# Kernel tuning notes

Measured on AMD Instinct MI355X. Metric: run time of the kernel, lower is better.

The kernel has to match this reference:

```python
import jax, jax.numpy as jnp
import numpy as np

N = 50000
D = 128
E = 640000


def _sage_conv(x, src, dst, w_self, w_neigh, b, n_nodes):
    # DGL SAGEConv(aggregator_type='mean'):
    #   h_neigh = mean_{u in N(v)} x_u ; out = x @ W_self + h_neigh @ W_neigh + b
    msg = x[src]                                          # [E, D] irregular gather
    s = jax.ops.segment_sum(msg, dst, num_segments=n_nodes)   # [N, D]
    deg = jax.ops.segment_sum(jnp.ones((src.shape[0],), dtype=x.dtype), dst,
                              num_segments=n_nodes)       # [N]
    h_neigh = jnp.where(deg[:, None] > 0, s / jnp.maximum(deg, 1.0)[:, None], 0.0)
    return x @ w_self + h_neigh @ w_neigh + b


def setup_inputs() -> dict:
    key = jax.random.key(0)
    ks = jax.random.split(key, 16)
    feat = jax.random.normal(ks[0], (N, D), dtype=jnp.float32)
    src = jax.random.randint(ks[1], (E,), 0, N, dtype=jnp.int32)
    dst = jax.random.randint(ks[2], (E,), 0, N, dtype=jnp.int32)
    etype = jax.random.randint(ks[3], (E,), 0, 4, dtype=jnp.int32)
    scale = 1.0 / np.sqrt(D)
    inp = {"feat": feat, "src": src, "dst": dst, "etype": etype}
    for i, name in enumerate(["1", "2", "3"]):
        inp[f"w_self{name}"] = jax.random.normal(ks[4 + 3 * i], (D, D), dtype=jnp.float32) * scale
        inp[f"w_neigh{name}"] = jax.random.normal(ks[5 + 3 * i], (D, D), dtype=jnp.float32) * scale
        inp[f"b{name}"] = jnp.zeros((D,), dtype=jnp.float32)
    return inp


def reference(feat, src, dst, etype,
              w_self1, w_neigh1, b1,
              w_self2, w_neigh2, b2,
              w_self3, w_neigh3, b3):
    n = feat.shape[0]
    h = _sage_conv(feat, src, dst, w_self1, w_neigh1, b1, n)
    h = jax.nn.relu(h) + feat
    h_prev = h
    h = _sage_conv(h, src, dst, w_self2, w_neigh2, b2, n)
    h = jax.nn.relu(h) + h_prev
    h_prev = h
    h = _sage_conv(h, src, dst, w_self3, w_neigh3, b3, n)
    h = jax.nn.relu(h) + h_prev
    return h
```

## Files before the change

### kernel.cpp

```cpp
#include <hip/hip_runtime.h>


#define DFEAT 128
#define BUCKET_CAP 64

typedef unsigned short ushort_t;
typedef unsigned int uint_t;
using short8  = __attribute__((ext_vector_type(8))) short;
using floatx4 = __attribute__((ext_vector_type(4))) float;

static __device__ __forceinline__ ushort_t f2bf(float f) {
    unsigned int u = __float_as_uint(f);
    u = (u + 0x7fffu + ((u >> 16) & 1u)) >> 16;
    return (ushort_t)u;
}
static __device__ __forceinline__ float bflo(uint_t v) {
    return __uint_as_float(v << 16);
}
static __device__ __forceinline__ float bfhi(uint_t v) {
    return __uint_as_float(v & 0xffff0000u);
}
static __device__ __forceinline__ float bf2f(ushort_t u) {
    return __uint_as_float((uint_t)u << 16);
}

__global__ void fill_buckets(const int* __restrict__ src, const int* __restrict__ dst,
                             int* __restrict__ cnt, ushort_t* __restrict__ bucket, int E) {
    int i = blockIdx.x * blockDim.x + threadIdx.x;
    if (i >= E) return;
    int d = dst[i];
    int slot = atomicAdd(&cnt[d], 1);
    if (slot < BUCKET_CAP) bucket[(size_t)d * BUCKET_CAP + slot] = (ushort_t)src[i];
}

__global__ __launch_bounds__(256) void prep_all(const float* __restrict__ w0,
                                                const float* __restrict__ w1,
                                                const float* __restrict__ w2,
                                                const float* __restrict__ w3,
                                                const float* __restrict__ w4,
                                                const float* __restrict__ w5,
                                                ushort_t* __restrict__ wt,
                                                const float* __restrict__ feat,
                                                ushort_t* __restrict__ featb,
                                                int* __restrict__ cnt,
                                                int n, int zb) {
    int b = blockIdx.x;
    if (b < zb) {
        int i = b * 1024 + threadIdx.x * 4;
        if (i < n) *(int4*)&cnt[i] = make_int4(0, 0, 0, 0);
        return;
    }
    b -= zb;
    if (b < 384) {
        const float* ws[6] = {w0, w1, w2, w3, w4, w5};
        const float* W = ws[b >> 6];
        ushort_t* O = wt + (size_t)(b >> 6) * DFEAT * DFEAT;
        int idx = (b & 63) * 256 + threadIdx.x;
        int k = idx >> 7, nn = idx & 127;
        O[nn * DFEAT + k] = f2bf(W[idx]);
        return;
    }
    b -= 384;
    int i = b * 256 + threadIdx.x;
    const float4* p = (const float4*)feat + (size_t)2 * i;
    float4 v0 = p[0], v1 = p[1];
    short8 u;
    u[0] = (short)f2bf(v0.x); u[1] = (short)f2bf(v0.y);
    u[2] = (short)f2bf(v0.z); u[3] = (short)f2bf(v0.w);
    u[4] = (short)f2bf(v1.x); u[5] = (short)f2bf(v1.y);
    u[6] = (short)f2bf(v1.z); u[7] = (short)f2bf(v1.w);
    *(short8*)&featb[(size_t)i * 8] = u;
}

__global__ __launch_bounds__(256) void aggregate(const ushort_t* __restrict__ xb,
                                                 const int* __restrict__ cnt,
                                                 const ushort_t* __restrict__ bucket,
                                                 ushort_t* __restrict__ outb, int n) {
    int node = (int)((blockIdx.x * blockDim.x + threadIdx.x) >> 6);
    int lane = threadIdx.x & 63;
    if (node >= n) return;
    int cn = cnt[node];
    int m = cn < BUCKET_CAP ? cn : BUCKET_CAP;
    const ushort_t* bk = bucket + (size_t)node * BUCKET_CAP;
    int myidx = (lane < m) ? (int)bk[lane] : 0;
    const uint_t* x1 = (const uint_t*)xb;

    float sx[8], sy[8];
#pragma unroll
    for (int j = 0; j < 8; ++j) { sx[j] = 0.f; sy[j] = 0.f; }

#pragma unroll 1
    for (int i = 0; i < m; i += 8) {
        int s[8];
#pragma unroll
        for (int j = 0; j < 8; ++j) s[j] = __shfl(myidx, i + j);
#pragma unroll
        for (int j = 1; j < 8; ++j) s[j] = (i + j < m) ? s[j] : s[0];
        uint_t v[8];
#pragma unroll
        for (int j = 0; j < 8; ++j) v[j] = x1[(size_t)s[j] * 64 + lane];
        sx[0] += bflo(v[0]); sy[0] += bfhi(v[0]);
#pragma unroll
        for (int j = 1; j < 8; ++j) {
            if (i + j < m) { sx[j] += bflo(v[j]); sy[j] += bfhi(v[j]); }
        }
    }
    float tx = ((sx[0] + sx[1]) + (sx[2] + sx[3])) + ((sx[4] + sx[5]) + (sx[6] + sx[7]));
    float ty = ((sy[0] + sy[1]) + (sy[2] + sy[3])) + ((sy[4] + sy[5]) + (sy[6] + sy[7]));
    float inv = cn > 0 ? 1.0f / (float)cn : 0.0f;
    uint_t o = ((uint_t)f2bf(ty * inv) << 16) | (uint_t)f2bf(tx * inv);
    ((uint_t*)outb)[(size_t)node * 64 + lane] = o;
}

__global__ __launch_bounds__(256) void sage_gemm_mfma(const ushort_t* __restrict__ xb,
                                                      const ushort_t* __restrict__ nbb,
                                                      const ushort_t* __restrict__ WsT,
                                                      const ushort_t* __restrict__ WnT,
                                                      const float* __restrict__ bias,
                                                      float* __restrict__ outf,
                                                      ushort_t* __restrict__ outb, int n) {
    __shared__ ushort_t As[64 * DFEAT];
    int t = threadIdx.x;
    int lane = t & 63;
    int w = t >> 6;
    int lr = lane & 15;
    int lg = lane >> 4;
    int row0 = blockIdx.x * 64;

    floatx4 acc[4][2];
#pragma unroll
    for (int m = 0; m < 4; ++m)
#pragma unroll
        for (int tt = 0; tt < 2; ++tt) acc[m][tt] = (floatx4)0.f;

#pragma unroll 1
    for (int phase = 0; phase < 2; ++phase) {
        const ushort_t* A = phase ? xb : nbb;
        const ushort_t* W = phase ? WsT : WnT;
        __syncthreads();
#pragma unroll
        for (int i = 0; i < 4; ++i) {
            int slot = i * 256 + t;
            int r = slot >> 4;
            int c = slot & 15;
            int gr = row0 + r;
            short8 u = (short8)0;
            if (gr < n) u = *(const short8*)&A[(size_t)gr * DFEAT + c * 8];
            int sc = c ^ (r & 7);
            *(short8*)&As[r * DFEAT + sc * 8] = u;
        }
        __syncthreads();
#pragma unroll
        for (int s = 0; s < 4; ++s) {
            short8 a[4], b[2];
#pragma unroll
            for (int m = 0; m < 4; ++m) {
                int r = m * 16 + lr;
                int c = s * 4 + lg;
                int sc = c ^ (r & 7);
                a[m] = *(const short8*)&As[r * DFEAT + sc * 8];
            }
#pragma unroll
            for (int tt = 0; tt < 2; ++tt) {
                int nn = w * 32 + tt * 16 + lr;
                b[tt] = *(const short8*)&W[(size_t)nn * DFEAT + s * 32 + lg * 8];
            }
#pragma unroll
            for (int m = 0; m < 4; ++m)
#pragma unroll
                for (int tt = 0; tt < 2; ++tt)
                    acc[m][tt] = __builtin_amdgcn_mfma_f32_16x16x32_bf16(
                        a[m], b[tt], acc[m][tt], 0, 0, 0);
        }
    }
#pragma unroll
    for (int tt = 0; tt < 2; ++tt) {
        int col = w * 32 + tt * 16 + lr;
        float bb = bias[col];
        int cch = col >> 3, cel = col & 7;
#pragma unroll
        for (int m = 0; m < 4; ++m) {
#pragma unroll
            for (int j = 0; j < 4; ++j) {
                int r = m * 16 + lg * 4 + j;
                int gr = row0 + r;
                if (gr < n) {
                    float xr = bf2f(As[r * DFEAT + (cch ^ (r & 7)) * 8 + cel]);
                    float v = fmaxf(acc[m][tt][j] + bb, 0.f) + xr;
                    if (outf) outf[(size_t)gr * DFEAT + col] = v;
                    if (outb) outb[(size_t)gr * DFEAT + col] = f2bf(v);
                }
            }
        }
    }
}

extern "C" void kernel_launch(void* const* d_in, const int* in_sizes, int n_in,
                              void* d_out, int out_size, void* d_ws, size_t ws_size,
                              hipStream_t stream) {
    const float* feat = (const float*)d_in[0];
    const int*   src  = (const int*)d_in[1];
    const int*   dst  = (const int*)d_in[2];
    const float* Ws1 = (const float*)d_in[4];
    const float* Wn1 = (const float*)d_in[5];
    const float* b1  = (const float*)d_in[6];
    const float* Ws2 = (const float*)d_in[7];
    const float* Wn2 = (const float*)d_in[8];
    const float* b2  = (const float*)d_in[9];
    const float* Ws3 = (const float*)d_in[10];
    const float* Wn3 = (const float*)d_in[11];
    const float* b3  = (const float*)d_in[12];

    int n = in_sizes[0] / DFEAT;
    int E = in_sizes[1];

    char* ws = (char*)d_ws;
    size_t off = 0;
    auto alloc = [&](size_t bytes) {
        size_t o = off;
        off = (off + bytes + 255) & ~(size_t)255;
        return o;
    };
    int*      cnt    = (int*)(ws + alloc((size_t)n * sizeof(int)));
    ushort_t* bucket = (ushort_t*)(ws + alloc((size_t)n * BUCKET_CAP * sizeof(ushort_t)));
    ushort_t* neighb = (ushort_t*)(ws + alloc((size_t)n * DFEAT * sizeof(ushort_t)));
    ushort_t* featb  = (ushort_t*)(ws + alloc((size_t)n * DFEAT * sizeof(ushort_t)));
    ushort_t* h1b    = (ushort_t*)(ws + alloc((size_t)n * DFEAT * sizeof(ushort_t)));
    ushort_t* Wt     = (ushort_t*)(ws + alloc((size_t)6 * DFEAT * DFEAT * sizeof(ushort_t)));
    ushort_t* h2b    = featb;
    (void)ws_size;

    ushort_t* Ws1T = Wt + 0 * DFEAT * DFEAT;
    ushort_t* Wn1T = Wt + 1 * DFEAT * DFEAT;
    ushort_t* Ws2T = Wt + 2 * DFEAT * DFEAT;
    ushort_t* Wn2T = Wt + 3 * DFEAT * DFEAT;
    ushort_t* Ws3T = Wt + 4 * DFEAT * DFEAT;
    ushort_t* Wn3T = Wt + 5 * DFEAT * DFEAT;

    float* outp = (float*)d_out;

    int zb = (n + 1023) / 1024;
    int cv = (n * DFEAT / 8 + 255) / 256;
    prep_all<<<zb + 384 + cv, 256, 0, stream>>>(Ws1, Wn1, Ws2, Wn2, Ws3, Wn3, Wt,
                                                feat, featb, cnt, n, zb);
    fill_buckets<<<(E + 255) / 256, 256, 0, stream>>>(src, dst, cnt, bucket, E);

    int agg_blocks  = (n + 3) / 4;
    int gemm_blocks = (n + 63) / 64;

    aggregate<<<agg_blocks, 256, 0, stream>>>(featb, cnt, bucket, neighb, n);
    sage_gemm_mfma<<<gemm_blocks, 256, 0, stream>>>(featb, neighb, Ws1T, Wn1T, b1,
                                                    nullptr, h1b, n);
    aggregate<<<agg_blocks, 256, 0, stream>>>(h1b, cnt, bucket, neighb, n);
    sage_gemm_mfma<<<gemm_blocks, 256, 0, stream>>>(h1b, neighb, Ws2T, Wn2T, b2,
                                                    nullptr, h2b, n);
    aggregate<<<agg_blocks, 256, 0, stream>>>(h2b, cnt, bucket, neighb, n);
    sage_gemm_mfma<<<gemm_blocks, 256, 0, stream>>>(h2b, neighb, Ws3T, Wn3T, b3,
                                                    outp, nullptr, n);
}
```

Baseline: 185.7 us.

## Build compact CSR adjacency and fuse mean aggregation into the MFMA GEMM kernel

Replaces fixed-capacity per-node buckets with a compact CSR built by histogram, wave-level scan with atomic range allocation, and scatter. Each GEMM block now gathers and averages neighbour features for its 64 rows directly into shared memory before running both MFMA products, removing the separate aggregate kernel and the neighbour-feature round trip through global memory. It also handles degrees above 64 exactly. In exchange, the gather runs with far fewer waves in flight (16 nodes per wave sequentially), and the CSR build adds an extra pass over the edges.

```diff
diff --git a/kernel.cpp b/kernel.cpp
--- a/kernel.cpp
+++ b/kernel.cpp
@@ -2,7 +2,6 @@
 
 
 #define DFEAT 128
-#define BUCKET_CAP 64
 
 typedef unsigned short ushort_t;
 typedef unsigned int uint_t;
@@ -14,24 +13,9 @@
     u = (u + 0x7fffu + ((u >> 16) & 1u)) >> 16;
     return (ushort_t)u;
 }
-static __device__ __forceinline__ float bflo(uint_t v) {
-    return __uint_as_float(v << 16);
-}
-static __device__ __forceinline__ float bfhi(uint_t v) {
-    return __uint_as_float(v & 0xffff0000u);
-}
-static __device__ __forceinline__ float bf2f(ushort_t u) {
-    return __uint_as_float((uint_t)u << 16);
-}
-
-__global__ void fill_buckets(const int* __restrict__ src, const int* __restrict__ dst,
-                             int* __restrict__ cnt, ushort_t* __restrict__ bucket, int E) {
-    int i = blockIdx.x * blockDim.x + threadIdx.x;
-    if (i >= E) return;
-    int d = dst[i];
-    int slot = atomicAdd(&cnt[d], 1);
-    if (slot < BUCKET_CAP) bucket[(size_t)d * BUCKET_CAP + slot] = (ushort_t)src[i];
-}
+static __device__ __forceinline__ float bflo(uint_t v) { return __uint_as_float(v << 16); }
+static __device__ __forceinline__ float bfhi(uint_t v) { return __uint_as_float(v & 0xffff0000u); }
+static __device__ __forceinline__ float bf2f(ushort_t u) { return __uint_as_float((uint_t)u << 16); }
 
 __global__ __launch_bounds__(256) void prep_all(const float* __restrict__ w0,
                                                 const float* __restrict__ w1,
@@ -43,11 +27,11 @@
                                                 const float* __restrict__ feat,
                                                 ushort_t* __restrict__ featb,
                                                 int* __restrict__ cnt,
-                                                int n, int zb) {
+                                                int nz, int zb) {
     int b = blockIdx.x;
     if (b < zb) {
         int i = b * 1024 + threadIdx.x * 4;
-        if (i < n) *(int4*)&cnt[i] = make_int4(0, 0, 0, 0);
+        if (i < nz) *(int4*)&cnt[i] = make_int4(0, 0, 0, 0);
         return;
     }
     b -= zb;
@@ -72,54 +56,54 @@
     *(short8*)&featb[(size_t)i * 8] = u;
 }
 
-__global__ __launch_bounds__(256) void aggregate(const ushort_t* __restrict__ xb,
-                                                 const int* __restrict__ cnt,
-                                                 const ushort_t* __restrict__ bucket,
-                                                 ushort_t* __restrict__ outb, int n) {
-    int node = (int)((blockIdx.x * blockDim.x + threadIdx.x) >> 6);
+__global__ void hist_k(const int* __restrict__ dst, int* __restrict__ cnt, int E) {
+    int i = blockIdx.x * blockDim.x + threadIdx.x;
+    if (i < E) atomicAdd(&cnt[dst[i]], 1);
+}
+
+__global__ __launch_bounds__(256) void alloc_ranges(const int* __restrict__ cnt,
+                                                    int2* __restrict__ meta,
+                                                    int* __restrict__ cursor,
+                                                    int* __restrict__ gcur, int n) {
+    int node = blockIdx.x * 256 + threadIdx.x;
     int lane = threadIdx.x & 63;
-    if (node >= n) return;
-    int cn = cnt[node];
-    int m = cn < BUCKET_CAP ? cn : BUCKET_CAP;
-    const ushort_t* bk = bucket + (size_t)node * BUCKET_CAP;
-    int myidx = (lane < m) ? (int)bk[lane] : 0;
-    const uint_t* x1 = (const uint_t*)xb;
-
-    float sx[8], sy[8];
-#pragma unroll
-    for (int j = 0; j < 8; ++j) { sx[j] = 0.f; sy[j] = 0.f; }
-
-#pragma unroll 1
-    for (int i = 0; i < m; i += 8) {
-        int s[8];
-#pragma unroll
-        for (int j = 0; j < 8; ++j) s[j] = __shfl(myidx, i + j);
-#pragma unroll
-        for (int j = 1; j < 8; ++j) s[j] = (i + j < m) ? s[j] : s[0];
-        uint_t v[8];
-#pragma unroll
-        for (int j = 0; j < 8; ++j) v[j] = x1[(size_t)s[j] * 64 + lane];
-        sx[0] += bflo(v[0]); sy[0] += bfhi(v[0]);
-#pragma unroll
-        for (int j = 1; j < 8; ++j) {
-            if (i + j < m) { sx[j] += bflo(v[j]); sy[j] += bfhi(v[j]); }
-        }
-    }
-    float tx = ((sx[0] + sx[1]) + (sx[2] + sx[3])) + ((sx[4] + sx[5]) + (sx[6] + sx[7]));
-    float ty = ((sy[0] + sy[1]) + (sy[2] + sy[3])) + ((sy[4] + sy[5]) + (sy[6] + sy[7]));
-    float inv = cn > 0 ? 1.0f / (float)cn : 0.0f;
-    uint_t o = ((uint_t)f2bf(ty * inv) << 16) | (uint_t)f2bf(tx * inv);
-    ((uint_t*)outb)[(size_t)node * 64 + lane] = o;
-}
-
-__global__ __launch_bounds__(256) void sage_gemm_mfma(const ushort_t* __restrict__ xb,
-                                                      const ushort_t* __restrict__ nbb,
-                                                      const ushort_t* __restrict__ WsT,
-                                                      const ushort_t* __restrict__ WnT,
-                                                      const float* __restrict__ bias,
-                                                      float* __restrict__ outf,
-                                                      ushort_t* __restrict__ outb, int n) {
+    int deg = (node < n) ? cnt[node] : 0;
+    int incl = deg;
+#pragma unroll
+    for (int d = 1; d < 64; d <<= 1) {
+        int v = __shfl_up(incl, d);
+        if (lane >= d) incl += v;
+    }
+    int total = __shfl(incl, 63);
+    int base = 0;
+    if (lane == 63 && total > 0) base = atomicAdd(gcur, total);
+    base = __shfl(base, 63);
+    int start = base + incl - deg;
+    if (node < n) {
+        meta[node] = make_int2(start, deg);
+        cursor[node] = start;
+    }
+}
+
+__global__ void scatter_csr(const int* __restrict__ src, const int* __restrict__ dst,
+                            int* __restrict__ cursor, ushort_t* __restrict__ csr, int E) {
+    int i = blockIdx.x * blockDim.x + threadIdx.x;
+    if (i >= E) return;
+    int d = dst[i];
+    int pos = atomicAdd(&cursor[d], 1);
+    csr[pos] = (ushort_t)src[i];
+}
+
+__global__ __launch_bounds__(256) void sage_fused(const ushort_t* __restrict__ xb,
+                                                  const int2* __restrict__ meta,
+                                                  const ushort_t* __restrict__ csr,
+                                                  const ushort_t* __restrict__ WsT,
+                                                  const ushort_t* __restrict__ WnT,
+                                                  const float* __restrict__ bias,
+                                                  float* __restrict__ outf,
+                                                  ushort_t* __restrict__ outb, int n) {
     __shared__ ushort_t As[64 * DFEAT];
+    __shared__ ushort_t Nb[64 * DFEAT];
     int t = threadIdx.x;
     int lane = t & 63;
     int w = t >> 6;
@@ -127,52 +111,122 @@
     int lg = lane >> 4;
     int row0 = blockIdx.x * 64;
 
+#pragma unroll
+    for (int i = 0; i < 4; ++i) {
+        int slot = i * 256 + t;
+        int r = slot >> 4;
+        int c = slot & 15;
+        int gr = row0 + r;
+        short8 u = (short8)0;
+        if (gr < n) u = *(const short8*)&xb[(size_t)gr * DFEAT + c * 8];
+        *(short8*)&As[r * DFEAT + (c ^ (r & 7)) * 8] = u;
+    }
+
+    const uint_t* x1 = (const uint_t*)xb;
+    int nbase = row0 + w * 16;
+    int cn_n = 0, bs_n = 0, ix_n = 0;
+    if (nbase < n) {
+        int2 md = meta[nbase];
+        cn_n = md.y; bs_n = md.x;
+        int mm = cn_n < 64 ? cn_n : 64;
+        ix_n = (lane < mm) ? (int)csr[bs_n + lane] : 0;
+    }
+#pragma unroll 1
+    for (int i = 0; i < 16; ++i) {
+        int node = nbase + i;
+        int cn = cn_n, base = bs_n, myidx = ix_n;
+        if (i < 15) {
+            int nd = node + 1;
+            cn_n = 0; bs_n = 0; ix_n = 0;
+            if (nd < n) {
+                int2 md = meta[nd];
+                cn_n = md.y; bs_n = md.x;
+                int mm = cn_n < 64 ? cn_n : 64;
+                ix_n = (lane < mm) ? (int)csr[bs_n + lane] : 0;
+            }
+        }
+        float tx = 0.f, ty = 0.f;
+        if (node < n && cn > 0) {
+            int m = cn < 64 ? cn : 64;
+            float sx[8], sy[8];
+#pragma unroll
+            for (int j = 0; j < 8; ++j) { sx[j] = 0.f; sy[j] = 0.f; }
+#pragma unroll 1
+            for (int ii = 0; ii < m; ii += 8) {
+                int s[8];
+#pragma unroll
+                for (int j = 0; j < 8; ++j) s[j] = __shfl(myidx, ii + j);
+#pragma unroll
+                for (int j = 1; j < 8; ++j) s[j] = (ii + j < m) ? s[j] : s[0];
+                uint_t v[8];
+#pragma unroll
+                for (int j = 0; j < 8; ++j) v[j] = x1[(size_t)s[j] * 64 + lane];
+                sx[0] += bflo(v[0]); sy[0] += bfhi(v[0]);
+#pragma unroll
+                for (int j = 1; j < 8; ++j) {
+                    if (ii + j < m) { sx[j] += bflo(v[j]); sy[j] += bfhi(v[j]); }
+                }
+            }
+            tx = ((sx[0] + sx[1]) + (sx[2] + sx[3])) + ((sx[4] + sx[5]) + (sx[6] + sx[7]));
+            ty = ((sy[0] + sy[1]) + (sy[2] + sy[3])) + ((sy[4] + sy[5]) + (sy[6] + sy[7]));
+            for (int ii = 64; ii < cn; ++ii) {
+                uint_t v = x1[(size_t)csr[base + ii] * 64 + lane];
+                tx += bflo(v); ty += bfhi(v);
+            }
+            float inv = 1.0f / (float)cn;
+            tx *= inv; ty *= inv;
+        }
+        int r = w * 16 + i;
+        int c = lane >> 2;
+        int e = (2 * lane) & 7;
+        uint_t o = ((uint_t)f2bf(ty) << 16) | (uint_t)f2bf(tx);
+        *(uint_t*)&Nb[r * DFEAT + (c ^ (r & 7)) * 8 + e] = o;
+    }
+    __syncthreads();
+
     floatx4 acc[4][2];
 #pragma unroll
     for (int m = 0; m < 4; ++m)
 #pragma unroll
         for (int tt = 0; tt < 2; ++tt) acc[m][tt] = (floatx4)0.f;
 
-#pragma unroll 1
-    for (int phase = 0; phase < 2; ++phase) {
-        const ushort_t* A = phase ? xb : nbb;
-        const ushort_t* W = phase ? WsT : WnT;
-        __syncthreads();
-#pragma unroll
-        for (int i = 0; i < 4; ++i) {
-            int slot = i * 256 + t;
-            int r = slot >> 4;
-            int c = slot & 15;
-            int gr = row0 + r;
-            short8 u = (short8)0;
-            if (gr < n) u = *(const short8*)&A[(size_t)gr * DFEAT + c * 8];
-            int sc = c ^ (r & 7);
-            *(short8*)&As[r * DFEAT + sc * 8] = u;
-        }
-        __syncthreads();
-#pragma unroll
-        for (int s = 0; s < 4; ++s) {
-            short8 a[4], b[2];
-#pragma unroll
-            for (int m = 0; m < 4; ++m) {
-                int r = m * 16 + lr;
-                int c = s * 4 + lg;
-                int sc = c ^ (r & 7);
-                a[m] = *(const short8*)&As[r * DFEAT + sc * 8];
-            }
-#pragma unroll
-            for (int tt = 0; tt < 2; ++tt) {
-                int nn = w * 32 + tt * 16 + lr;
-                b[tt] = *(const short8*)&W[(size_t)nn * DFEAT + s * 32 + lg * 8];
-            }
-#pragma unroll
-            for (int m = 0; m < 4; ++m)
-#pragma unroll
-                for (int tt = 0; tt < 2; ++tt)
-                    acc[m][tt] = __builtin_amdgcn_mfma_f32_16x16x32_bf16(
-                        a[m], b[tt], acc[m][tt], 0, 0, 0);
-        }
-    }
+#pragma unroll
+    for (int s = 0; s < 4; ++s) {
+        short8 a[4], b[2];
+#pragma unroll
+        for (int m = 0; m < 4; ++m) {
+            int r = m * 16 + lr;
+            int c = s * 4 + lg;
+            a[m] = *(const short8*)&Nb[r * DFEAT + (c ^ (r & 7)) * 8];
+        }
+#pragma unroll
+        for (int tt = 0; tt < 2; ++tt) {
+            int nn = w * 32 + tt * 16 + lr;
+            b[tt] = *(const short8*)&WnT[(size_t)nn * DFEAT + s * 32 + lg * 8];
+        }
+#pragma unroll
+        for (int m = 0; m < 4; ++m)
+#pragma unroll
+            for (int tt = 0; tt < 2; ++tt)
+                acc[m][tt] = __builtin_amdgcn_mfma_f32_16x16x32_bf16(a[m], b[tt], acc[m][tt], 0, 0, 0);
+#pragma unroll
+        for (int m = 0; m < 4; ++m) {
+            int r = m * 16 + lr;
+            int c = s * 4 + lg;
+            a[m] = *(const short8*)&As[r * DFEAT + (c ^ (r & 7)) * 8];
+        }
+#pragma unroll
+        for (int tt = 0; tt < 2; ++tt) {
+            int nn = w * 32 + tt * 16 + lr;
+            b[tt] = *(const short8*)&WsT[(size_t)nn * DFEAT + s * 32 + lg * 8];
+        }
+#pragma unroll
+        for (int m = 0; m < 4; ++m)
+#pragma unroll
+            for (int tt = 0; tt < 2; ++tt)
+                acc[m][tt] = __builtin_amdgcn_mfma_f32_16x16x32_bf16(a[m], b[tt], acc[m][tt], 0, 0, 0);
+    }
+
 #pragma unroll
     for (int tt = 0; tt < 2; ++tt) {
         int col = w * 32 + tt * 16 + lr;
@@ -221,13 +275,16 @@
         off = (off + bytes + 255) & ~(size_t)255;
         return o;
     };
-    int*      cnt    = (int*)(ws + alloc((size_t)n * sizeof(int)));
-    ushort_t* bucket = (ushort_t*)(ws + alloc((size_t)n * BUCKET_CAP * sizeof(ushort_t)));
-    ushort_t* neighb = (ushort_t*)(ws + alloc((size_t)n * DFEAT * sizeof(ushort_t)));
+    int nz = n + 64;
+    int*      cnt    = (int*)(ws + alloc((size_t)nz * sizeof(int)));
+    int2*     meta   = (int2*)(ws + alloc((size_t)n * sizeof(int2)));
+    int*      cursor = (int*)(ws + alloc((size_t)n * sizeof(int)));
+    ushort_t* csr    = (ushort_t*)(ws + alloc((size_t)E * sizeof(ushort_t)));
     ushort_t* featb  = (ushort_t*)(ws + alloc((size_t)n * DFEAT * sizeof(ushort_t)));
     ushort_t* h1b    = (ushort_t*)(ws + alloc((size_t)n * DFEAT * sizeof(ushort_t)));
     ushort_t* Wt     = (ushort_t*)(ws + alloc((size_t)6 * DFEAT * DFEAT * sizeof(ushort_t)));
     ushort_t* h2b    = featb;
+    int*      gcur   = cnt + n;
     (void)ws_size;
 
     ushort_t* Ws1T = Wt + 0 * DFEAT * DFEAT;
@@ -239,22 +296,19 @@
 
     float* outp = (float*)d_out;
 
-    int zb = (n + 1023) / 1024;
+    int zb = (nz + 1023) / 1024;
     int cv = (n * DFEAT / 8 + 255) / 256;
     prep_all<<<zb + 384 + cv, 256, 0, stream>>>(Ws1, Wn1, Ws2, Wn2, Ws3, Wn3, Wt,
-                                                feat, featb, cnt, n, zb);
-    fill_buckets<<<(E + 255) / 256, 256, 0, stream>>>(src, dst, cnt, bucket, E);
-
-    int agg_blocks  = (n + 3) / 4;
+                                                feat, featb, cnt, nz, zb);
+    hist_k<<<(E + 255) / 256, 256, 0, stream>>>(dst, cnt, E);
+    alloc_ranges<<<(n + 255) / 256, 256, 0, stream>>>(cnt, meta, cursor, gcur, n);
+    scatter_csr<<<(E + 255) / 256, 256, 0, stream>>>(src, dst, cursor, csr, E);
+
     int gemm_blocks = (n + 63) / 64;
-
-    aggregate<<<agg_blocks, 256, 0, stream>>>(featb, cnt, bucket, neighb, n);
-    sage_gemm_mfma<<<gemm_blocks, 256, 0, stream>>>(featb, neighb, Ws1T, Wn1T, b1,
-                                                    nullptr, h1b, n);
-    aggregate<<<agg_blocks, 256, 0, stream>>>(h1b, cnt, bucket, neighb, n);
-    sage_gemm_mfma<<<gemm_blocks, 256, 0, stream>>>(h1b, neighb, Ws2T, Wn2T, b2,
-                                                    nullptr, h2b, n);
-    aggregate<<<agg_blocks, 256, 0, stream>>>(h2b, cnt, bucket, neighb, n);
-    sage_gemm_mfma<<<gemm_blocks, 256, 0, stream>>>(h2b, neighb, Ws3T, Wn3T, b3,
-                                                    outp, nullptr, n);
-}
+    sage_fused<<<gemm_blocks, 256, 0, stream>>>(featb, meta, csr, Ws1T, Wn1T, b1,
+                                                nullptr, h1b, n);
+    sage_fused<<<gemm_blocks, 256, 0, stream>>>(h1b, meta, csr, Ws2T, Wn2T, b2,
+                                                nullptr, h2b, n);
+    sage_fused<<<gemm_blocks, 256, 0, stream>>>(h2b, meta, csr, Ws3T, Wn3T, b3,
+                                                outp, nullptr, n);
+}
```

Result: slower. 376.1 us (+102.6%).

## Replace fixed-capacity neighbor buckets with compact CSR built via histogram and scan

Applied to the files above, without the earlier changes.

Builds a compact CSR adjacency using a degree histogram, a wave-level prefix scan with atomic range allocation, and an atomic scatter of source ids. Aggregation reads neighbor ids from contiguous CSR ranges and handles degrees beyond 64 with a tail loop, removing the old bucket truncation. This shrinks the adjacency footprint but adds two extra kernel launches and a second atomic pass over the edges.

```diff
diff --git a/kernel.cpp b/kernel.cpp
--- a/kernel.cpp
+++ b/kernel.cpp
@@ -2,7 +2,6 @@
 
 
 #define DFEAT 128
-#define BUCKET_CAP 64
 
 typedef unsigned short ushort_t;
 typedef unsigned int uint_t;
@@ -14,24 +13,9 @@
     u = (u + 0x7fffu + ((u >> 16) & 1u)) >> 16;
     return (ushort_t)u;
 }
-static __device__ __forceinline__ float bflo(uint_t v) {
-    return __uint_as_float(v << 16);
-}
-static __device__ __forceinline__ float bfhi(uint_t v) {
-    return __uint_as_float(v & 0xffff0000u);
-}
-static __device__ __forceinline__ float bf2f(ushort_t u) {
-    return __uint_as_float((uint_t)u << 16);
-}
-
-__global__ void fill_buckets(const int* __restrict__ src, const int* __restrict__ dst,
-                             int* __restrict__ cnt, ushort_t* __restrict__ bucket, int E) {
-    int i = blockIdx.x * blockDim.x + threadIdx.x;
-    if (i >= E) return;
-    int d = dst[i];
-    int slot = atomicAdd(&cnt[d], 1);
-    if (slot < BUCKET_CAP) bucket[(size_t)d * BUCKET_CAP + slot] = (ushort_t)src[i];
-}
+static __device__ __forceinline__ float bflo(uint_t v) { return __uint_as_float(v << 16); }
+static __device__ __forceinline__ float bfhi(uint_t v) { return __uint_as_float(v & 0xffff0000u); }
+static __device__ __forceinline__ float bf2f(ushort_t u) { return __uint_as_float((uint_t)u << 16); }
 
 __global__ __launch_bounds__(256) void prep_all(const float* __restrict__ w0,
                                                 const float* __restrict__ w1,
@@ -43,11 +27,11 @@
                                                 const float* __restrict__ feat,
                                                 ushort_t* __restrict__ featb,
                                                 int* __restrict__ cnt,
-                                                int n, int zb) {
+                                                int nz, int zb) {
     int b = blockIdx.x;
     if (b < zb) {
         int i = b * 1024 + threadIdx.x * 4;
-        if (i < n) *(int4*)&cnt[i] = make_int4(0, 0, 0, 0);
+        if (i < nz) *(int4*)&cnt[i] = make_int4(0, 0, 0, 0);
         return;
     }
     b -= zb;
@@ -72,17 +56,55 @@
     *(short8*)&featb[(size_t)i * 8] = u;
 }
 
+__global__ void hist_k(const int* __restrict__ dst, int* __restrict__ cnt, int E) {
+    int i = blockIdx.x * blockDim.x + threadIdx.x;
+    if (i < E) atomicAdd(&cnt[dst[i]], 1);
+}
+
+__global__ __launch_bounds__(256) void alloc_ranges(const int* __restrict__ cnt,
+                                                    int2* __restrict__ meta,
+                                                    int* __restrict__ cursor,
+                                                    int* __restrict__ gcur, int n) {
+    int node = blockIdx.x * 256 + threadIdx.x;
+    int lane = threadIdx.x & 63;
+    int deg = (node < n) ? cnt[node] : 0;
+    int incl = deg;
+#pragma unroll
+    for (int d = 1; d < 64; d <<= 1) {
+        int v = __shfl_up(incl, d);
+        if (lane >= d) incl += v;
+    }
+    int total = __shfl(incl, 63);
+    int base = 0;
+    if (lane == 63 && total > 0) base = atomicAdd(gcur, total);
+    base = __shfl(base, 63);
+    int start = base + incl - deg;
+    if (node < n) {
+        meta[node] = make_int2(start, deg);
+        cursor[node] = start;
+    }
+}
+
+__global__ void scatter_csr(const int* __restrict__ src, const int* __restrict__ dst,
+                            int* __restrict__ cursor, ushort_t* __restrict__ csr, int E) {
+    int i = blockIdx.x * blockDim.x + threadIdx.x;
+    if (i >= E) return;
+    int d = dst[i];
+    int pos = atomicAdd(&cursor[d], 1);
+    csr[pos] = (ushort_t)src[i];
+}
+
 __global__ __launch_bounds__(256) void aggregate(const ushort_t* __restrict__ xb,
-                                                 const int* __restrict__ cnt,
-                                                 const ushort_t* __restrict__ bucket,
+                                                 const int2* __restrict__ meta,
+                                                 const ushort_t* __restrict__ csr,
                                                  ushort_t* __restrict__ outb, int n) {
     int node = (int)((blockIdx.x * blockDim.x + threadIdx.x) >> 6);
     int lane = threadIdx.x & 63;
     if (node >= n) return;
-    int cn = cnt[node];
-    int m = cn < BUCKET_CAP ? cn : BUCKET_CAP;
-    const ushort_t* bk = bucket + (size_t)node * BUCKET_CAP;
-    int myidx = (lane < m) ? (int)bk[lane] : 0;
+    int2 md = meta[node];
+    int base = md.x, cn = md.y;
+    int m = cn < 64 ? cn : 64;
+    int myidx = (lane < m) ? (int)csr[base + lane] : 0;
     const uint_t* x1 = (const uint_t*)xb;
 
     float sx[8], sy[8];
@@ -107,6 +129,11 @@
     }
     float tx = ((sx[0] + sx[1]) + (sx[2] + sx[3])) + ((sx[4] + sx[5]) + (sx[6] + sx[7]));
     float ty = ((sy[0] + sy[1]) + (sy[2] + sy[3])) + ((sy[4] + sy[5]) + (sy[6] + sy[7]));
+#pragma unroll 1
+    for (int ii = 64; ii < cn; ++ii) {
+        uint_t v = x1[(size_t)csr[base + ii] * 64 + lane];
+        tx += bflo(v); ty += bfhi(v);
+    }
     float inv = cn > 0 ? 1.0f / (float)cn : 0.0f;
     uint_t o = ((uint_t)f2bf(ty * inv) << 16) | (uint_t)f2bf(tx * inv);
     ((uint_t*)outb)[(size_t)node * 64 + lane] = o;
@@ -146,8 +173,7 @@
             int gr = row0 + r;
             short8 u = (short8)0;
             if (gr < n) u = *(const short8*)&A[(size_t)gr * DFEAT + c * 8];
-            int sc = c ^ (r & 7);
-            *(short8*)&As[r * DFEAT + sc * 8] = u;
+            *(short8*)&As[r * DFEAT + (c ^ (r & 7)) * 8] = u;
         }
         __syncthreads();
 #pragma unroll
@@ -157,8 +183,7 @@
             for (int m = 0; m < 4; ++m) {
                 int r = m * 16 + lr;
                 int c = s * 4 + lg;
-                int sc = c ^ (r & 7);
-                a[m] = *(const short8*)&As[r * DFEAT + sc * 8];
+                a[m] = *(const short8*)&As[r * DFEAT + (c ^ (r & 7)) * 8];
             }
 #pragma unroll
             for (int tt = 0; tt < 2; ++tt) {
@@ -221,13 +246,17 @@
         off = (off + bytes + 255) & ~(size_t)255;
         return o;
     };
-    int*      cnt    = (int*)(ws + alloc((size_t)n * sizeof(int)));
-    ushort_t* bucket = (ushort_t*)(ws + alloc((size_t)n * BUCKET_CAP * sizeof(ushort_t)));
-    ushort_t* neighb = (ushort_t*)(ws + alloc((size_t)n * DFEAT * sizeof(ushort_t)));
+    int nz = n + 64;
+    int*      cnt    = (int*)(ws + alloc((size_t)nz * sizeof(int)));
+    int2*     meta   = (int2*)(ws + alloc((size_t)n * sizeof(int2)));
+    int*      cursor = (int*)(ws + alloc((size_t)n * sizeof(int)));
+    ushort_t* csr    = (ushort_t*)(ws + alloc((size_t)E * sizeof(ushort_t)));
     ushort_t* featb  = (ushort_t*)(ws + alloc((size_t)n * DFEAT * sizeof(ushort_t)));
     ushort_t* h1b    = (ushort_t*)(ws + alloc((size_t)n * DFEAT * sizeof(ushort_t)));
+    ushort_t* neighb = (ushort_t*)(ws + alloc((size_t)n * DFEAT * sizeof(ushort_t)));
     ushort_t* Wt     = (ushort_t*)(ws + alloc((size_t)6 * DFEAT * DFEAT * sizeof(ushort_t)));
     ushort_t* h2b    = featb;
+    int*      gcur   = cnt + n;
     (void)ws_size;
 
     ushort_t* Ws1T = Wt + 0 * DFEAT * DFEAT;
@@ -239,22 +268,24 @@
 
     float* outp = (float*)d_out;
 
-    int zb = (n + 1023) / 1024;
+    int zb = (nz + 1023) / 1024;
     int cv = (n * DFEAT / 8 + 255) / 256;
     prep_all<<<zb + 384 + cv, 256, 0, stream>>>(Ws1, Wn1, Ws2, Wn2, Ws3, Wn3, Wt,
-                                                feat, featb, cnt, n, zb);
-    fill_buckets<<<(E + 255) / 256, 256, 0, stream>>>(src, dst, cnt, bucket, E);
+                                                feat, featb, cnt, nz, zb);
+    hist_k<<<(E + 255) / 256, 256, 0, stream>>>(dst, cnt, E);
+    alloc_ranges<<<(n + 255) / 256, 256, 0, stream>>>(cnt, meta, cursor, gcur, n);
+    scatter_csr<<<(E + 255) / 256, 256, 0, stream>>>(src, dst, cursor, csr, E);
 
     int agg_blocks  = (n + 3) / 4;
     int gemm_blocks = (n + 63) / 64;
 
-    aggregate<<<agg_blocks, 256, 0, stream>>>(featb, cnt, bucket, neighb, n);
+    aggregate<<<agg_blocks, 256, 0, stream>>>(featb, meta, csr, neighb, n);
     sage_gemm_mfma<<<gemm_blocks, 256, 0, stream>>>(featb, neighb, Ws1T, Wn1T, b1,
                                                     nullptr, h1b, n);
-    aggregate<<<agg_blocks, 256, 0, stream>>>(h1b, cnt, bucket, neighb, n);
+    aggregate<<<agg_blocks, 256, 0, stream>>>(h1b, meta, csr, neighb, n);
     sage_gemm_mfma<<<gemm_blocks, 256, 0, stream>>>(h1b, neighb, Ws2T, Wn2T, b2,
                                                     nullptr, h2b, n);
-    aggregate<<<agg_blocks, 256, 0, stream>>>(h2b, cnt, bucket, neighb, n);
+    aggregate<<<agg_blocks, 256, 0, stream>>>(h2b, meta, csr, neighb, n);
     sage_gemm_mfma<<<gemm_blocks, 256, 0, stream>>>(h2b, neighb, Ws3T, Wn3T, b3,
                                                     outp, nullptr, n);
 }
```

After: 222.9 us. +20.1%, slower.
